# Kernel tuning notes

Measured on AMD Instinct MI355X. Metric: run time of the kernel, lower is better.

Reference implementation:

```python
import jax, jax.numpy as jnp
import numpy as np

J = 116  # ROI count; c_in = 4*J = 464


def setup_inputs() -> dict:
    key = jax.random.key(0)
    ks = jax.random.split(key, 8)
    B = 131072
    F = jax.random.normal(ks[0], (B, 2, J), dtype=jnp.float32)
    S = jax.random.normal(ks[1], (B, 2, J), dtype=jnp.float32)
    def lin(k, fan_in, fan_out):
        bound = 1.0 / np.sqrt(fan_in)
        kw, kb = jax.random.split(k)
        W = jax.random.uniform(kw, (fan_in, fan_out), jnp.float32, -bound, bound)
        b = jax.random.uniform(kb, (fan_out,), jnp.float32, -bound, bound)
        return W, b
    W1, b1 = lin(ks[2], 4 * J, 64)
    W2, b2 = lin(ks[3], 64, 32)
    W3, b3 = lin(ks[4], 32, 2)
    return {"F": F, "S": S, "W1": W1, "b1": b1, "W2": W2, "b2": b2, "W3": W3, "b3": b3}


def reference(F, S, W1, b1, W2, b2, W3, b3):
    # einsum('bkj,bij->bjki') then mean over (k,i) factors into mean_k(F)*mean_i(S)
    # per (b,j): mean_{k,i} F[b,k,j]*S[b,i,j] = mean_k F[b,k,j] * mean_i S[b,i,j]
    g = jax.nn.sigmoid(jnp.mean(F, axis=1) * jnp.mean(S, axis=1))  # (b, j)
    g = g[:, None, :]                                              # broadcast over the 2 channels
    Fg = F * g
    Sg = S * g
    feat = jnp.concatenate((Fg, Sg), axis=1).reshape(F.shape[0], -1)  # (b, 4*J)
    h = jax.nn.relu(feat @ W1 + b1)
    h = jax.nn.relu(h @ W2 + b2)
    logits = h @ W3 + b3
    return jax.nn.softmax(logits, axis=1)
```

## Files before the change

### kernel.cpp

```cpp
#include <hip/hip_runtime.h>
#include <stdint.h>


typedef float     f4    __attribute__((ext_vector_type(4)));
typedef float     f32x4 __attribute__((ext_vector_type(4)));
typedef _Float16  h4    __attribute__((ext_vector_type(4)));
typedef _Float16  h8    __attribute__((ext_vector_type(8)));

#define NSTEP 15
#define LDA   488

__global__ void prep_w1(const float* __restrict__ W1, _Float16* __restrict__ Wsp) {
  const int e  = blockIdx.x * 256 + threadIdx.x;
  const int t  = e >> 11;
  const int r  = e & 2047;
  const int n  = r & 63;
  const int kk = r >> 6;
  const int k  = t * 32 + kk;
  const float v = (k < 464) ? W1[k * 64 + n] : 0.f;
  Wsp[t * 2048 + n * 32 + kk] = (_Float16)v;
}

__global__ __launch_bounds__(256, 2) void mricls_main(
    const float* __restrict__ F, const float* __restrict__ S,
    const float* __restrict__ b1, const float* __restrict__ W2,
    const float* __restrict__ b2, const float* __restrict__ W3,
    const float* __restrict__ b3, const _Float16* __restrict__ Wsp,
    float* __restrict__ out) {
  __shared__ __align__(16) union {
    _Float16 A16[64 * LDA];
    float    h1[64][68];
  } U;
  __shared__ __align__(16) float W2s[64][32];
  __shared__ __align__(16) float W3s[32][2];
  __shared__ __align__(16) float b1s[64];
  __shared__ __align__(16) float b2s[32];
  __shared__ float b3s[2];

  const int tid = threadIdx.x;

  {
    const f4* W2v = (const f4*)W2;
    f4* W2sv = (f4*)W2s;
#pragma unroll
    for (int i = 0; i < 2; ++i) W2sv[tid + 256 * i] = W2v[tid + 256 * i];
    if (tid < 16) ((f4*)W3s)[tid] = ((const f4*)W3)[tid];
    if (tid < 16) ((f4*)b1s)[tid] = ((const f4*)b1)[tid];
    if (tid < 8)  ((f4*)b2s)[tid] = ((const f4*)b2)[tid];
    if (tid < 2)  b3s[tid] = b3[tid];
  }

  {
    const int zr = tid >> 2;
    const int zk = 464 + (tid & 3) * 4;
    *(h4*)(U.A16 + zr * LDA + zk) = (h4){0, 0, 0, 0};
  }

  {
    const int  row = tid >> 2;
    const int  c   = tid & 3;
    const long grow = (long)blockIdx.x * 64 + row;
    const float* fr = F + grow * 232;
    const float* sr = S + grow * 232;
#pragma unroll
    for (int i = 0; i < 8; ++i) {
      const int q = c + 4 * i;
      if (q < 29) {
        const f4 f0 = *(const f4*)(fr + 4 * q);
        const f4 f1 = *(const f4*)(fr + 4 * q + 116);
        const f4 s0 = *(const f4*)(sr + 4 * q);
        const f4 s1 = *(const f4*)(sr + 4 * q + 116);
        h4 a0, a1, a2, a3;
#pragma unroll
        for (int e = 0; e < 4; ++e) {
          const float x = 0.25f * (f0[e] + f1[e]) * (s0[e] + s1[e]);
          const float g = 1.f / (1.f + __expf(-x));
          a0[e] = (_Float16)(f0[e] * g);
          a1[e] = (_Float16)(f1[e] * g);
          a2[e] = (_Float16)(s0[e] * g);
          a3[e] = (_Float16)(s1[e] * g);
        }
        _Float16* base = U.A16 + row * LDA + 4 * q;
        *(h4*)(base)       = a0;
        *(h4*)(base + 116) = a1;
        *(h4*)(base + 232) = a2;
        *(h4*)(base + 348) = a3;
      }
    }
  }
  __syncthreads();

  const int l  = tid & 63;
  const int w  = tid >> 6;
  const int ml = l & 15;
  const int h  = l >> 4;

  f32x4 acc[4];
#pragma unroll
  for (int nt = 0; nt < 4; ++nt) acc[nt] = (f32x4){0.f, 0.f, 0.f, 0.f};

  const _Float16* Arow  = U.A16 + (w * 16 + ml) * LDA + 8 * h;
  const _Float16* Bbase = Wsp + ml * 32 + 8 * h;
#pragma unroll
  for (int t = 0; t < NSTEP; ++t) {
    const h8 a = *(const h8*)(Arow + 32 * t);
#pragma unroll
    for (int nt = 0; nt < 4; ++nt) {
      const h8 b = *(const h8*)(Bbase + t * 2048 + nt * 512);
      acc[nt] = __builtin_amdgcn_mfma_f32_16x16x32_f16(a, b, acc[nt], 0, 0, 0);
    }
  }
  __syncthreads();

#pragma unroll
  for (int nt = 0; nt < 4; ++nt) {
    const int n = nt * 16 + ml;
    const float bias = b1s[n];
#pragma unroll
    for (int r = 0; r < 4; ++r) {
      const int mm = w * 16 + h * 4 + r;
      U.h1[mm][n] = fmaxf(acc[nt][r] + bias, 0.f);
    }
  }
  __syncthreads();

  const int m2 = tid >> 2;
  const int q  = tid & 3;
  float acc2[8];
#pragma unroll
  for (int e = 0; e < 8; ++e) acc2[e] = b2s[q * 8 + e];
#pragma unroll 8
  for (int k = 0; k < 64; ++k) {
    const float hk = U.h1[m2][k];
    const f4 w0 = *(const f4*)&W2s[k][q * 8];
    const f4 w1 = *(const f4*)&W2s[k][q * 8 + 4];
    acc2[0] = fmaf(hk, w0[0], acc2[0]);
    acc2[1] = fmaf(hk, w0[1], acc2[1]);
    acc2[2] = fmaf(hk, w0[2], acc2[2]);
    acc2[3] = fmaf(hk, w0[3], acc2[3]);
    acc2[4] = fmaf(hk, w1[0], acc2[4]);
    acc2[5] = fmaf(hk, w1[1], acc2[5]);
    acc2[6] = fmaf(hk, w1[2], acc2[6]);
    acc2[7] = fmaf(hk, w1[3], acc2[7]);
  }
  float p0 = 0.f, p1 = 0.f;
#pragma unroll
  for (int e = 0; e < 8; ++e) {
    const float hv = fmaxf(acc2[e], 0.f);
    p0 = fmaf(hv, W3s[q * 8 + e][0], p0);
    p1 = fmaf(hv, W3s[q * 8 + e][1], p1);
  }
  p0 += __shfl_xor(p0, 1); p0 += __shfl_xor(p0, 2);
  p1 += __shfl_xor(p1, 1); p1 += __shfl_xor(p1, 2);
  if (q == 0) {
    const float l0 = p0 + b3s[0], l1 = p1 + b3s[1];
    const float mx = fmaxf(l0, l1);
    const float e0 = __expf(l0 - mx), e1 = __expf(l1 - mx);
    const float inv = 1.f / (e0 + e1);
    float2 o = make_float2(e0 * inv, e1 * inv);
    *(float2*)(out + ((long)blockIdx.x * 64 + m2) * 2) = o;
  }
}

extern "C" void kernel_launch(void* const* d_in, const int* in_sizes, int n_in,
                              void* d_out, int out_size, void* d_ws, size_t ws_size,
                              hipStream_t stream) {
  const float* F  = (const float*)d_in[0];
  const float* S  = (const float*)d_in[1];
  const float* W1 = (const float*)d_in[2];
  const float* b1 = (const float*)d_in[3];
  const float* W2 = (const float*)d_in[4];
  const float* b2 = (const float*)d_in[5];
  const float* W3 = (const float*)d_in[6];
  const float* b3 = (const float*)d_in[7];
  _Float16* Wsp = (_Float16*)d_ws;
  float* out = (float*)d_out;
  const int B = in_sizes[0] / 232;

  prep_w1<<<dim3(120), dim3(256), 0, stream>>>(W1, Wsp);
  mricls_main<<<dim3(B / 64), dim3(256), 0, stream>>>(F, S, b1, W2, b2, W3, b3,
                                                      (const _Float16*)Wsp, out);
}
```

Baseline: 311.2 us.

## Build MFMA A operands directly from global loads, dropping the LDS staging tile

The activation tile is no longer staged in LDS. Each MFMA lane now loads F/S values straight from global memory in the K order the operand needs, computes the sigmoid gate with a cross-half lane shuffle to pair the F and S channel sums, and converts to fp16 in registers. W1 is re-permuted in the prep kernel so its K dimension matches this interleaved (channel, ROI) order. Cutting the ~61KB LDS buffer lets the launch bound rise to 4 blocks per CU, aiming for more occupancy and one fewer barrier. The cost is extra loads for the paired channel, redundant sigmoid evaluation across lanes, and less coalesced global access.

```diff
diff --git a/kernel.cpp b/kernel.cpp
--- a/kernel.cpp
+++ b/kernel.cpp
@@ -2,13 +2,11 @@
 #include <stdint.h>
 
 
-typedef float     f4    __attribute__((ext_vector_type(4)));
-typedef float     f32x4 __attribute__((ext_vector_type(4)));
-typedef _Float16  h4    __attribute__((ext_vector_type(4)));
-typedef _Float16  h8    __attribute__((ext_vector_type(8)));
+typedef float    f4    __attribute__((ext_vector_type(4)));
+typedef float    f32x4 __attribute__((ext_vector_type(4)));
+typedef _Float16 h8    __attribute__((ext_vector_type(8)));
 
 #define NSTEP 15
-#define LDA   488
 
 __global__ void prep_w1(const float* __restrict__ W1, _Float16* __restrict__ Wsp) {
   const int e  = blockIdx.x * 256 + threadIdx.x;
@@ -16,21 +14,19 @@
   const int r  = e & 2047;
   const int n  = r & 63;
   const int kk = r >> 6;
-  const int k  = t * 32 + kk;
-  const float v = (k < 464) ? W1[k * 64 + n] : 0.f;
+  const int q  = kk >> 3;
+  const int j  = 8 * t + (kk & 7);
+  const float v = (j < 116) ? W1[(116 * q + j) * 64 + n] : 0.f;
   Wsp[t * 2048 + n * 32 + kk] = (_Float16)v;
 }
 
-__global__ __launch_bounds__(256, 2) void mricls_main(
+__global__ __launch_bounds__(256, 4) void mricls_main(
     const float* __restrict__ F, const float* __restrict__ S,
     const float* __restrict__ b1, const float* __restrict__ W2,
     const float* __restrict__ b2, const float* __restrict__ W3,
     const float* __restrict__ b3, const _Float16* __restrict__ Wsp,
     float* __restrict__ out) {
-  __shared__ __align__(16) union {
-    _Float16 A16[64 * LDA];
-    float    h1[64][68];
-  } U;
+  __shared__ __align__(16) float h1s[64][68];
   __shared__ __align__(16) float W2s[64][32];
   __shared__ __align__(16) float W3s[32][2];
   __shared__ __align__(16) float b1s[64];
@@ -38,6 +34,10 @@
   __shared__ float b3s[2];
 
   const int tid = threadIdx.x;
+  const int l   = tid & 63;
+  const int w   = tid >> 6;
+  const int ml  = l & 15;
+  const int h   = l >> 4;
 
   {
     const f4* W2v = (const f4*)W2;
@@ -50,66 +50,47 @@
     if (tid < 2)  b3s[tid] = b3[tid];
   }
 
-  {
-    const int zr = tid >> 2;
-    const int zk = 464 + (tid & 3) * 4;
-    *(h4*)(U.A16 + zr * LDA + zk) = (h4){0, 0, 0, 0};
-  }
-
-  {
-    const int  row = tid >> 2;
-    const int  c   = tid & 3;
-    const long grow = (long)blockIdx.x * 64 + row;
-    const float* fr = F + grow * 232;
-    const float* sr = S + grow * 232;
-#pragma unroll
-    for (int i = 0; i < 8; ++i) {
-      const int q = c + 4 * i;
-      if (q < 29) {
-        const f4 f0 = *(const f4*)(fr + 4 * q);
-        const f4 f1 = *(const f4*)(fr + 4 * q + 116);
-        const f4 s0 = *(const f4*)(sr + 4 * q);
-        const f4 s1 = *(const f4*)(sr + 4 * q + 116);
-        h4 a0, a1, a2, a3;
-#pragma unroll
-        for (int e = 0; e < 4; ++e) {
-          const float x = 0.25f * (f0[e] + f1[e]) * (s0[e] + s1[e]);
-          const float g = 1.f / (1.f + __expf(-x));
-          a0[e] = (_Float16)(f0[e] * g);
-          a1[e] = (_Float16)(f1[e] * g);
-          a2[e] = (_Float16)(s0[e] * g);
-          a3[e] = (_Float16)(s1[e] * g);
-        }
-        _Float16* base = U.A16 + row * LDA + 4 * q;
-        *(h4*)(base)       = a0;
-        *(h4*)(base + 116) = a1;
-        *(h4*)(base + 232) = a2;
-        *(h4*)(base + 348) = a3;
-      }
-    }
-  }
-  __syncthreads();
-
-  const int l  = tid & 63;
-  const int w  = tid >> 6;
-  const int ml = l & 15;
-  const int h  = l >> 4;
+  const long row = (long)blockIdx.x * 64 + w * 16 + ml;
+  const float* arr   = (h < 2) ? F : S;
+  const float* base  = arr + row * 232 + ((h & 1) ? 116 : 0);
+  const float* pbase = arr + row * 232 + ((h & 1) ? 0 : 116);
+  const _Float16* Bb = Wsp + ml * 32 + 8 * h;
 
   f32x4 acc[4];
 #pragma unroll
   for (int nt = 0; nt < 4; ++nt) acc[nt] = (f32x4){0.f, 0.f, 0.f, 0.f};
 
-  const _Float16* Arow  = U.A16 + (w * 16 + ml) * LDA + 8 * h;
-  const _Float16* Bbase = Wsp + ml * 32 + 8 * h;
 #pragma unroll
   for (int t = 0; t < NSTEP; ++t) {
-    const h8 a = *(const h8*)(Arow + 32 * t);
+    const f4 x0 = *(const f4*)(base  + 8 * t);
+    const f4 p0 = *(const f4*)(pbase + 8 * t);
+    f4 x1, p1;
+    if (t < NSTEP - 1) {
+      x1 = *(const f4*)(base  + 8 * t + 4);
+      p1 = *(const f4*)(pbase + 8 * t + 4);
+    } else {
+      x1 = (f4){0.f, 0.f, 0.f, 0.f};
+      p1 = (f4){0.f, 0.f, 0.f, 0.f};
+    }
+    h8 a;
+#pragma unroll
+    for (int e = 0; e < 4; ++e) {
+      const float u0 = x0[e] + p0[e];
+      const float u1 = x1[e] + p1[e];
+      const float v0 = __shfl_xor(u0, 32);
+      const float v1 = __shfl_xor(u1, 32);
+      const float g0 = 1.f / (1.f + __expf(-0.25f * u0 * v0));
+      const float g1 = 1.f / (1.f + __expf(-0.25f * u1 * v1));
+      a[e]     = (_Float16)(x0[e] * g0);
+      a[e + 4] = (_Float16)(x1[e] * g1);
+    }
 #pragma unroll
     for (int nt = 0; nt < 4; ++nt) {
-      const h8 b = *(const h8*)(Bbase + t * 2048 + nt * 512);
+      const h8 b = *(const h8*)(Bb + t * 2048 + nt * 512);
       acc[nt] = __builtin_amdgcn_mfma_f32_16x16x32_f16(a, b, acc[nt], 0, 0, 0);
     }
   }
+
   __syncthreads();
 
 #pragma unroll
@@ -119,7 +100,7 @@
 #pragma unroll
     for (int r = 0; r < 4; ++r) {
       const int mm = w * 16 + h * 4 + r;
-      U.h1[mm][n] = fmaxf(acc[nt][r] + bias, 0.f);
+      h1s[mm][n] = fmaxf(acc[nt][r] + bias, 0.f);
     }
   }
   __syncthreads();
@@ -131,7 +112,7 @@
   for (int e = 0; e < 8; ++e) acc2[e] = b2s[q * 8 + e];
 #pragma unroll 8
   for (int k = 0; k < 64; ++k) {
-    const float hk = U.h1[m2][k];
+    const float hk = h1s[m2][k];
     const f4 w0 = *(const f4*)&W2s[k][q * 8];
     const f4 w1 = *(const f4*)&W2s[k][q * 8 + 4];
     acc2[0] = fmaf(hk, w0[0], acc2[0]);
```

Result: slower. 407.0 us (+30.8%).
